# Kernel tuning notes

Measured on AMD Instinct MI355X. Metric: run time of the kernel, lower is better.

## Reference

```python
import jax, jax.numpy as jnp
import numpy as np

CUTOFFS = [16000, 28000, 36000]
HID = 1024
PROJ = [256, 64]  # hidden/4**1, hidden/4**2 per compute_proj_dims
CLUSTERS = 2


def setup_inputs() -> dict:
    key = jax.random.key(0)
    ks = jax.random.split(key, 12)
    B, S = 4, 1024
    scale = 0.02
    d = {
        "inp": jax.random.normal(ks[0], (B, S, HID), jnp.float32),
        "labels": jax.random.randint(ks[1], (B, S), 0, CUTOFFS[-1]),
        "head_W": jax.random.normal(ks[2], (HID, CUTOFFS[0] + CLUSTERS), jnp.float32) * scale,
        "head_b": jnp.zeros((CUTOFFS[0] + CLUSTERS,), jnp.float32),
    }
    for i in range(CLUSTERS):
        tdim = CUTOFFS[i + 1] - CUTOFFS[i]
        d[f"t{i}_pW"] = jax.random.normal(ks[3 + 4 * i], (HID, PROJ[i]), jnp.float32) * scale
        d[f"t{i}_pb"] = jnp.zeros((PROJ[i],), jnp.float32)
        d[f"t{i}_W"] = jax.random.normal(ks[4 + 4 * i], (PROJ[i], CUTOFFS[i + 1] - CUTOFFS[i]), jnp.float32) * scale
        d[f"t{i}_b"] = jnp.zeros((CUTOFFS[i + 1] - CUTOFFS[i],), jnp.float32)
    return d


def _sparse_ce(logits, labels):
    # stable sparse softmax cross entropy, single log_softmax pass
    logp = jax.nn.log_softmax(logits, axis=-1)
    return -jnp.take_along_axis(logp, labels[..., None], axis=-1)[..., 0]


def reference(inp, labels, head_W, head_b, t0_pW, t0_pb, t0_W, t0_b, t1_pW, t1_pb, t1_W, t1_b):
    tails = [(t0_pW, t0_pb, t0_W, t0_b), (t1_pW, t1_pb, t1_W, t1_b)]
    head_labels = labels
    loss = jnp.zeros(labels.shape, inp.dtype)
    for i, (pW, pb, W, b) in enumerate(tails):
        lo, hi = CUTOFFS[i], CUTOFFS[i + 1]
        mask = (labels >= lo) & (labels < hi)
        # tokens in cluster i are relabeled to cluster id in the head
        head_labels = jnp.where(mask, CUTOFFS[0] + i, head_labels)
        # two-layer tail projection: [B,S,H] -> [B,S,proj] -> [B,S,tail_dim]
        tail_logits = (inp @ pW + pb) @ W + b
        tail_labels = jnp.clip(labels - lo, 0, hi - lo - 1)
        loss = loss + jnp.where(mask, _sparse_ce(tail_logits, tail_labels), 0.0)
    head_logits = inp @ head_W + head_b  # [B,S,cutoffs[0]+clusters]
    loss = _sparse_ce(head_logits, head_labels) + loss
    loss = loss * (labels != 0).astype(loss.dtype)  # zero out pad positions
    return jnp.mean(loss)
```

## Files before the change

kernel.cpp:

```cpp
#include <hip/hip_runtime.h>
#include <hip/hip_bf16.h>
#include <hip/hip_fp8.h>
#include <cstdint>
#include <cstddef>

#define M_TOK 4096
#define HID   1024
#define NHEAD 16002
#define NHEAD_PAD 16128
#define P0    256
#define N0    12000
#define N0_PAD 12032
#define P1    64
#define N1    8000
#define N1_PAD 8192
#define PFUSE 384
#define PREAL 320

typedef unsigned char u8;
typedef float f32x4 __attribute__((ext_vector_type(4)));
typedef int   i32x4 __attribute__((ext_vector_type(4)));
typedef int   i32x8 __attribute__((ext_vector_type(8)));

__device__ __forceinline__ void load16(const void* g, void* l) {
    __builtin_amdgcn_global_load_lds(
        (__attribute__((address_space(1))) void*)g,
        (__attribute__((address_space(3))) void*)l,
        16, 0, 0);
}

__device__ __forceinline__ u8 to_e4m3(float f) {
    __hip_fp8_e4m3 h(f);
    return (u8)h.__x;
}

union Frag { struct { i32x4 lo, hi; } half; i32x8 v; };

struct Seg {
    const u8* A; int lda;
    const u8* BT; int ldb;
    const float* bias; int K; int realN;
    const int* tgt; float* sumexp; float* lab;
    int nblk;
};

__launch_bounds__(512, 4)
__global__ void gemm_lse3(Seg s0, Seg s1, Seg s2) {
    __shared__ __align__(16) u8 As[32768];
    __shared__ __align__(16) u8 Bs[16384];

    int b = blockIdx.x;
    Seg sg; int rel;
    if (b < s0.nblk)                { sg = s0; rel = b; }
    else if (b < s0.nblk + s1.nblk) { sg = s1; rel = b - s0.nblk; }
    else                            { sg = s2; rel = b - s0.nblk - s1.nblk; }
    int pair = rel >> 5, inner = rel & 31;
    int m0 = (inner >> 1) * 256;
    int n0 = (pair * 2 + (inner & 1)) * 128;

    const int lda = sg.lda, ldb = sg.ldb;
    const int tid  = threadIdx.x;
    const int lane = tid & 63;
    const int wave = tid >> 6;
    const int wm = wave >> 1, wn = wave & 1;
    const int q = lane >> 4, lrow = lane & 15;
    const int sw = lrow & 7;

    int aofs[4], abase[4], bofs[2], bbase[2];
    #pragma unroll
    for (int p = 0; p < 4; p++) {
        int pg = wave * 256 + p * 64 + lane;
        int row = pg >> 3, gcol = (pg & 7) ^ (row & 7);
        aofs[p]  = row * lda + gcol * 16;
        abase[p] = (wave * 256 + p * 64) * 16;
    }
    #pragma unroll
    for (int p = 0; p < 2; p++) {
        int pg = wave * 128 + p * 64 + lane;
        int row = pg >> 3, gcol = (pg & 7) ^ (row & 7);
        bofs[p]  = row * ldb + gcol * 16;
        bbase[p] = (wave * 128 + p * 64) * 16;
    }

    f32x4 acc[4][4];
    #pragma unroll
    for (int mt = 0; mt < 4; mt++)
        #pragma unroll
        for (int nt = 0; nt < 4; nt++)
            acc[mt][nt] = (f32x4)(0.0f);

    const u8* Ab = sg.A  + (size_t)m0 * lda;
    const u8* Bb = sg.BT + (size_t)n0 * ldb;

    const int aLo = ((wm * 64 + lrow) * 8 + ((2 * q)     ^ sw)) * 16;
    const int aHi = ((wm * 64 + lrow) * 8 + ((2 * q + 1) ^ sw)) * 16;
    const int bLo = ((wn * 64 + lrow) * 8 + ((2 * q)     ^ sw)) * 16;
    const int bHi = ((wn * 64 + lrow) * 8 + ((2 * q + 1) ^ sw)) * 16;

    for (int k0 = 0; k0 < sg.K; k0 += 128) {
        #pragma unroll
        for (int p = 0; p < 4; p++)
            load16(Ab + k0 + aofs[p], As + abase[p]);
        #pragma unroll
        for (int p = 0; p < 2; p++)
            load16(Bb + k0 + bofs[p], Bs + bbase[p]);
        __syncthreads();

        Frag fb[4];
        #pragma unroll
        for (int t = 0; t < 4; t++) {
            fb[t].half.lo = *reinterpret_cast<const i32x4*>(Bs + bLo + t * 2048);
            fb[t].half.hi = *reinterpret_cast<const i32x4*>(Bs + bHi + t * 2048);
        }
        Frag fa[2];
        fa[0].half.lo = *reinterpret_cast<const i32x4*>(As + aLo);
        fa[0].half.hi = *reinterpret_cast<const i32x4*>(As + aHi);
        #pragma unroll
        for (int mt = 0; mt < 4; mt++) {
            if (mt < 3) {
                fa[(mt + 1) & 1].half.lo = *reinterpret_cast<const i32x4*>(As + aLo + (mt + 1) * 2048);
                fa[(mt + 1) & 1].half.hi = *reinterpret_cast<const i32x4*>(As + aHi + (mt + 1) * 2048);
            }
            #pragma unroll
            for (int nt = 0; nt < 4; nt++)
                acc[mt][nt] = __builtin_amdgcn_mfma_scale_f32_16x16x128_f8f6f4(
                    fa[mt & 1].v, fb[nt].v, acc[mt][nt],
                    0, 0,
                    0, 0x7F7F7F7F,
                    0, 0x7A7A7A7A);
        }
        __syncthreads();
    }

    int colg[4]; float bias_v[4];
    #pragma unroll
    for (int nt = 0; nt < 4; nt++) {
        colg[nt] = n0 + wn * 64 + nt * 16 + lrow;
        bias_v[nt] = (colg[nt] < sg.realN) ? sg.bias[colg[nt]] : 0.0f;
    }

    float* sred = reinterpret_cast<float*>(As);

    #pragma unroll
    for (int mt = 0; mt < 4; mt++) {
        int rloc = wm * 64 + mt * 16 + q * 4;
        #pragma unroll
        for (int r = 0; r < 4; r++) {
            int tok = m0 + rloc + r;
            int tg = sg.tgt[tok];
            float ps = 0.0f;
            #pragma unroll
            for (int nt = 0; nt < 4; nt++) {
                if (colg[nt] < sg.realN) {
                    float logit = acc[mt][nt][r] + bias_v[nt];
                    ps += __expf(logit);
                    if (colg[nt] == tg) atomicAdd(&sg.lab[tok], logit);
                }
            }
            ps += __shfl_xor(ps, 1);
            ps += __shfl_xor(ps, 2);
            ps += __shfl_xor(ps, 4);
            ps += __shfl_xor(ps, 8);
            if (lrow == 0) sred[wn * 256 + rloc + r] = ps;
        }
    }
    __syncthreads();
    if (tid < 256) {
        float v = sred[tid] + sred[256 + tid];
        atomicAdd(&sg.sumexp[m0 + tid], v);
    }
}

__device__ __forceinline__ void proj_body(const u8* __restrict__ A, const u8* __restrict__ BT,
                                          const float* __restrict__ bias, u8* __restrict__ out,
                                          int m0, int n0, u8* As, u8* Bs) {
    const int lda = HID, ldb = HID, ldo = PFUSE;
    const int tid  = threadIdx.x;
    const int lane = tid & 63;
    const int wave = tid >> 6;
    const int wm = wave >> 2, wn = wave & 3;
    const int q = lane >> 4, lrow = lane & 15;
    const int sw = lrow & 7;

    int aofs[2], bofs[2], lbase[2];
    #pragma unroll
    for (int p = 0; p < 2; p++) {
        int pg = wave * 128 + p * 64 + lane;
        int row = pg >> 3, gcol = (pg & 7) ^ (row & 7);
        aofs[p]  = row * lda + gcol * 16;
        bofs[p]  = row * ldb + gcol * 16;
        lbase[p] = (wave * 128 + p * 64) * 16;
    }

    f32x4 acc[4][2];
    #pragma unroll
    for (int mt = 0; mt < 4; mt++)
        #pragma unroll
        for (int nt = 0; nt < 2; nt++)
            acc[mt][nt] = (f32x4)(0.0f);

    const u8* Ab = A  + (size_t)m0 * lda;
    const u8* Bb = BT + (size_t)n0 * ldb;

    const int aLo = ((wm * 64 + lrow) * 8 + ((2 * q)     ^ sw)) * 16;
    const int aHi = ((wm * 64 + lrow) * 8 + ((2 * q + 1) ^ sw)) * 16;
    const int bLo = ((wn * 32 + lrow) * 8 + ((2 * q)     ^ sw)) * 16;
    const int bHi = ((wn * 32 + lrow) * 8 + ((2 * q + 1) ^ sw)) * 16;

    for (int k0 = 0; k0 < HID; k0 += 128) {
        #pragma unroll
        for (int p = 0; p < 2; p++) {
            load16(Ab + k0 + aofs[p], As + lbase[p]);
            load16(Bb + k0 + bofs[p], Bs + lbase[p]);
        }
        __syncthreads();
        Frag fb[2];
        #pragma unroll
        for (int t = 0; t < 2; t++) {
            fb[t].half.lo = *reinterpret_cast<const i32x4*>(Bs + bLo + t * 2048);
            fb[t].half.hi = *reinterpret_cast<const i32x4*>(Bs + bHi + t * 2048);
        }
        #pragma unroll
        for (int mt = 0; mt < 4; mt++) {
            Frag fa;
            fa.half.lo = *reinterpret_cast<const i32x4*>(As + aLo + mt * 2048);
            fa.half.hi = *reinterpret_cast<const i32x4*>(As + aHi + mt * 2048);
            #pragma unroll
            for (int nt = 0; nt < 2; nt++)
                acc[mt][nt] = __builtin_amdgcn_mfma_scale_f32_16x16x128_f8f6f4(
                    fa.v, fb[nt].v, acc[mt][nt],
                    0, 0, 0, 0x7F7F7F7F, 0, 0x7A7A7A7A);
        }
        __syncthreads();
    }

    int colg[2]; float bias_v[2];
    #pragma unroll
    for (int nt = 0; nt < 2; nt++) {
        colg[nt] = n0 + wn * 32 + nt * 16 + lrow;
        bias_v[nt] = (colg[nt] < PREAL) ? bias[colg[nt]] : 0.0f;
    }
    #pragma unroll
    for (int mt = 0; mt < 4; mt++) {
        int rowb = m0 + wm * 64 + mt * 16 + q * 4;
        #pragma unroll
        for (int r = 0; r < 4; r++) {
            int tok = rowb + r;
            #pragma unroll
            for (int nt = 0; nt < 2; nt++)
                out[(size_t)tok * ldo + colg[nt]] = to_e4m3(acc[mt][nt][r] + bias_v[nt]);
        }
    }
}

__device__ __forceinline__ void do_transpose512(const float* __restrict__ W, u8* __restrict__ WT,
                                                int K, int N, int Kpad, float scale,
                                                int bx, int by, float (*tile)[65]) {
    int n0 = bx * 64, k0 = by * 64;
    int c2 = threadIdx.x & 31;
    int rg = threadIdx.x >> 5;
    int n = n0 + c2 * 2;
    #pragma unroll
    for (int j = 0; j < 4; j++) {
        int k = k0 + rg + j * 16;
        float2 v;
        if (k < K && n + 1 < N) {
            v = *reinterpret_cast<const float2*>(&W[(size_t)k * N + n]);
        } else {
            v.x = (k < K && n     < N) ? W[(size_t)k * N + n]     : 0.0f;
            v.y = (k < K && n + 1 < N) ? W[(size_t)k * N + n + 1] : 0.0f;
        }
        tile[rg + j * 16][c2 * 2]     = v.x * scale;
        tile[rg + j * 16][c2 * 2 + 1] = v.y * scale;
    }
    __syncthreads();
    int nn = threadIdx.x >> 3, kb = (threadIdx.x & 7) * 8;
    union { u8 b[8]; uint2 u; } v;
    #pragma unroll
    for (int j = 0; j < 8; j++) v.b[j] = to_e4m3(tile[kb + j][nn]);
    *reinterpret_cast<uint2*>(WT + (size_t)(n0 + nn) * Kpad + k0 + kb) = v.u;
}

#define P1_CAST 512
#define P1_T0P   64
#define P1_T1P   32
#define P1_INIT   8

__global__ void prep1_kernel(const float* __restrict__ inp, const int* __restrict__ labels,
                             const float* __restrict__ t0_pW, const float* __restrict__ t0_pb,
                             const float* __restrict__ t1_pW, const float* __restrict__ t1_pb,
                             u8* __restrict__ inp_f8, u8* __restrict__ fpW8,
                             float* __restrict__ acc6, int* __restrict__ tgts,
                             float* __restrict__ pbias, float* __restrict__ out) {
    __shared__ float tile[64][65];
    int b = blockIdx.x;
    if (b < P1_CAST) {
        int i = b * 512 + threadIdx.x;
        float4 v = reinterpret_cast<const float4*>(inp)[i];
        uchar4 o8;
        o8.x = to_e4m3(v.x); o8.y = to_e4m3(v.y); o8.z = to_e4m3(v.z); o8.w = to_e4m3(v.w);
        reinterpret_cast<uchar4*>(inp_f8)[i] = o8;
    } else if (b < P1_CAST + P1_T0P) {
        int r = b - P1_CAST;
        do_transpose512(t0_pW, fpW8, HID, P0, HID, 32.0f, r % 4, r / 4, tile);
    } else if (b < P1_CAST + P1_T0P + P1_T1P) {
        int r = b - (P1_CAST + P1_T0P);
        do_transpose512(t1_pW, fpW8 + 256 * HID, HID, P1, HID, 32.0f, r % 2, r / 2, tile);
    } else {
        int r = b - (P1_CAST + P1_T0P + P1_T1P);
        int t = r * 512 + threadIdx.x;
        for (int j = t; j < 6 * M_TOK; j += M_TOK) acc6[j] = 0.0f;
        if (t == 0) out[0] = 0.0f;
        if (t < PFUSE) pbias[t] = (t < 256) ? t0_pb[t] : ((t < PREAL) ? t1_pb[t - 256] : 0.0f);
        int lbl = labels[t];
        tgts[t]             = (lbl < 16000) ? lbl : ((lbl < 28000) ? 16000 : 16001);
        int t0 = lbl - 16000; t0 = t0 < 0 ? 0 : (t0 > 11999 ? 11999 : t0);
        int t1 = lbl - 28000; t1 = t1 < 0 ? 0 : (t1 > 7999  ? 7999  : t1);
        tgts[M_TOK + t]     = t0;
        tgts[2 * M_TOK + t] = t1;
    }
}

#define P2_HEAD 4032
#define P2_T0W   752
#define P2_T1W   256
#define P2_PROJ   96

__launch_bounds__(512, 4)
__global__ void prep2_kernel(const float* __restrict__ head_W,
                             const float* __restrict__ t0_W, const float* __restrict__ t1_W,
                             const u8* __restrict__ inp_f8, const u8* __restrict__ fpW8,
                             const float* __restrict__ pbias,
                             u8* __restrict__ headW8, u8* __restrict__ t0W8,
                             u8* __restrict__ t1W8, u8* __restrict__ proj8) {
    __shared__ __align__(16) u8 smem[32768];
    int b = blockIdx.x;
    if (b < P2_HEAD) {
        do_transpose512(head_W, headW8, HID, NHEAD, HID, 32.0f, b % 252, b / 252,
                        reinterpret_cast<float (*)[65]>(smem));
    } else if (b < P2_HEAD + P2_T0W) {
        int r = b - P2_HEAD;
        do_transpose512(t0_W, t0W8, P0, N0, P0, 32.0f, r % 188, r / 188,
                        reinterpret_cast<float (*)[65]>(smem));
    } else if (b < P2_HEAD + P2_T0W + P2_T1W) {
        int r = b - (P2_HEAD + P2_T0W);
        do_transpose512(t1_W, t1W8, P1, N1, 128, 32.0f, r % 128, r / 128,
                        reinterpret_cast<float (*)[65]>(smem));
    } else {
        int r = b - (P2_HEAD + P2_T0W + P2_T1W);
        int m0 = (r & 31) * 128;
        int n0 = (r >> 5) * 128;
        proj_body(inp_f8, fpW8, pbias, proj8, m0, n0, smem, smem + 16384);
    }
}

__global__ void finalize_kernel(const int* __restrict__ labels, const float* __restrict__ acc6,
                                float* __restrict__ out) {
    int t = blockIdx.x * blockDim.x + threadIdx.x;
    const float* sumH = acc6;
    const float* labH = acc6 + M_TOK;
    const float* sum0 = acc6 + 2 * M_TOK;
    const float* lab0 = acc6 + 3 * M_TOK;
    const float* sum1 = acc6 + 4 * M_TOK;
    const float* lab1 = acc6 + 5 * M_TOK;
    int lbl = labels[t];
    float l = 0.0f;
    if (lbl != 0) {
        l = logf(sumH[t]) - labH[t];
        if (lbl >= 16000 && lbl < 28000) l += logf(sum0[t]) - lab0[t];
        else if (lbl >= 28000)           l += logf(sum1[t]) - lab1[t];
    }
    l *= (1.0f / (float)M_TOK);
    #pragma unroll
    for (int off = 1; off < 64; off <<= 1) l += __shfl_xor(l, off);
    __shared__ float red[4];
    if ((threadIdx.x & 63) == 0) red[threadIdx.x >> 6] = l;
    __syncthreads();
    if (threadIdx.x == 0) atomicAdd(out, red[0] + red[1] + red[2] + red[3]);
}

extern "C" void kernel_launch(void* const* d_in, const int* in_sizes, int n_in,
                              void* d_out, int out_size, void* d_ws, size_t ws_size,
                              hipStream_t stream) {
    const float* inp    = (const float*)d_in[0];
    const int*   labels = (const int*)  d_in[1];
    const float* head_W = (const float*)d_in[2];
    const float* head_b = (const float*)d_in[3];
    const float* t0_pW  = (const float*)d_in[4];
    const float* t0_pb  = (const float*)d_in[5];
    const float* t0_W   = (const float*)d_in[6];
    const float* t0_b   = (const float*)d_in[7];
    const float* t1_pW  = (const float*)d_in[8];
    const float* t1_pb  = (const float*)d_in[9];
    const float* t1_W   = (const float*)d_in[10];
    const float* t1_b   = (const float*)d_in[11];
    float* out = (float*)d_out;

    char* ws = (char*)d_ws;
    size_t off = 0;
    auto alloc = [&](size_t bytes) { char* p = ws + off; off += (bytes + 255) & ~(size_t)255; return p; };
    u8*    inp_f8  = (u8*)   alloc((size_t)M_TOK * HID);
    u8*    headW8  = (u8*)   alloc((size_t)NHEAD_PAD * HID);
    u8*    fpW8    = (u8*)   alloc((size_t)PFUSE * HID);
    u8*    t0W8    = (u8*)   alloc((size_t)N0_PAD * P0);
    u8*    t1W8    = (u8*)   alloc((size_t)N1_PAD * 128);
    u8*    proj8   = (u8*)   alloc((size_t)M_TOK * PFUSE);
    float* acc6    = (float*)alloc(6 * M_TOK * 4);
    int*   tgts    = (int*)  alloc(3 * M_TOK * 4);
    float* pbias   = (float*)alloc(PFUSE * 4);

    prep1_kernel<<<P1_CAST + P1_T0P + P1_T1P + P1_INIT, 512, 0, stream>>>(
        inp, labels, t0_pW, t0_pb, t1_pW, t1_pb,
        inp_f8, fpW8, acc6, tgts, pbias, out);

    prep2_kernel<<<P2_HEAD + P2_T0W + P2_T1W + P2_PROJ, 512, 0, stream>>>(
        head_W, t0_W, t1_W, inp_f8, fpW8, pbias,
        headW8, t0W8, t1W8, proj8);

    Seg s0{inp_f8,      HID,   headW8, HID, head_b, HID, NHEAD, tgts,             acc6,             acc6 + M_TOK,     16 * (NHEAD_PAD / 128)};
    Seg s1{proj8,       PFUSE, t0W8,   P0,  t0_b,   P0,  N0,    tgts + M_TOK,     acc6 + 2 * M_TOK, acc6 + 3 * M_TOK, 16 * (N0_PAD / 128)};
    Seg s2{proj8 + 256, PFUSE, t1W8,   128, t1_b,   128, N1,    tgts + 2 * M_TOK, acc6 + 4 * M_TOK, acc6 + 5 * M_TOK, 16 * (N1_PAD / 128)};
    gemm_lse3<<<s0.nblk + s1.nblk + s2.nblk, 512, 0, stream>>>(s0, s1, s2);

    finalize_kernel<<<M_TOK / 256, 256, 0, stream>>>(labels, acc6, out);
}
```

Before: 301.5 us.

## Fuse finalize into GEMM via last-block reduction and use packed fp8 conversion

The separate finalize kernel is removed. Each GEMM block now bumps a global counter after its atomics, and whichever block finishes last computes the loss reduction and writes the output. The transpose-and-cast helper now converts to fp8 before staging through LDS, using packed hardware cvt_pk_fp8 intrinsics, with larger tiles of 128 k by 64 n and half the block count. This aims to save one kernel launch and cut LDS traffic and conversion instructions in the prep kernels, at the cost of a fence plus a global atomic per GEMM block.

After: 897.9 us. 2.98x slower.

```diff
diff --git a/kernel.cpp b/kernel.cpp
--- a/kernel.cpp
+++ b/kernel.cpp
@@ -1,6 +1,5 @@
 #include <hip/hip_runtime.h>
 #include <hip/hip_bf16.h>
-#include <hip/hip_fp8.h>
 #include <cstdint>
 #include <cstddef>
 
@@ -30,8 +29,16 @@
 }
 
 __device__ __forceinline__ u8 to_e4m3(float f) {
-    __hip_fp8_e4m3 h(f);
-    return (u8)h.__x;
+    return (u8)(__builtin_amdgcn_cvt_pk_fp8_f32(f, f, 0, false) & 0xff);
+}
+__device__ __forceinline__ unsigned cvt4(float x, float y, float z, float w) {
+    int r = __builtin_amdgcn_cvt_pk_fp8_f32(x, y, 0, false);
+    r = __builtin_amdgcn_cvt_pk_fp8_f32(z, w, r, true);
+    return (unsigned)r;
+}
+
+__device__ __forceinline__ float aload(const float* p) {
+    return __hip_atomic_load(p, __ATOMIC_RELAXED, __HIP_MEMORY_SCOPE_AGENT);
 }
 
 union Frag { struct { i32x4 lo, hi; } half; i32x8 v; };
@@ -45,7 +52,9 @@
 };
 
 __launch_bounds__(512, 4)
-__global__ void gemm_lse3(Seg s0, Seg s1, Seg s2) {
+__global__ void gemm_lse3(Seg s0, Seg s1, Seg s2,
+                          const int* __restrict__ labels, float* __restrict__ acc6,
+                          int* __restrict__ cnt, float* __restrict__ out, int nblkTotal) {
     __shared__ __align__(16) u8 As[32768];
     __shared__ __align__(16) u8 Bs[16384];
 
@@ -169,6 +178,40 @@
         float v = sred[tid] + sred[256 + tid];
         atomicAdd(&sg.sumexp[m0 + tid], v);
     }
+
+    __threadfence();
+    __shared__ int lastBlk;
+    __syncthreads();
+    if (tid == 0) {
+        int old = __hip_atomic_fetch_add(cnt, 1, __ATOMIC_ACQ_REL, __HIP_MEMORY_SCOPE_AGENT);
+        lastBlk = (old == nblkTotal - 1) ? 1 : 0;
+    }
+    __syncthreads();
+    if (lastBlk) {
+        float part = 0.0f;
+        for (int t = tid; t < M_TOK; t += 512) {
+            int lbl = labels[t];
+            if (lbl != 0) {
+                float l = logf(aload(&acc6[t])) - aload(&acc6[M_TOK + t]);
+                if (lbl >= 16000 && lbl < 28000)
+                    l += logf(aload(&acc6[2 * M_TOK + t])) - aload(&acc6[3 * M_TOK + t]);
+                else if (lbl >= 28000)
+                    l += logf(aload(&acc6[4 * M_TOK + t])) - aload(&acc6[5 * M_TOK + t]);
+                part += l;
+            }
+        }
+        #pragma unroll
+        for (int o = 1; o < 64; o <<= 1) part += __shfl_xor(part, o);
+        float* red = reinterpret_cast<float*>(Bs);
+        if ((tid & 63) == 0) red[tid >> 6] = part;
+        __syncthreads();
+        if (tid == 0) {
+            float s = 0.0f;
+            #pragma unroll
+            for (int i = 0; i < 8; i++) s += red[i];
+            out[0] = s * (1.0f / (float)M_TOK);
+        }
+    }
 }
 
 __device__ __forceinline__ void proj_body(const u8* __restrict__ A, const u8* __restrict__ BT,
@@ -253,37 +296,44 @@
     }
 }
 
-__device__ __forceinline__ void do_transpose512(const float* __restrict__ W, u8* __restrict__ WT,
-                                                int K, int N, int Kpad, float scale,
-                                                int bx, int by, float (*tile)[65]) {
-    int n0 = bx * 64, k0 = by * 64;
-    int c2 = threadIdx.x & 31;
-    int rg = threadIdx.x >> 5;
-    int n = n0 + c2 * 2;
+__device__ __forceinline__ void tr_cast(const float* __restrict__ W, u8* __restrict__ WT,
+                                        int K, int N, int Kpad, float scale,
+                                        int bx, int by, u8* ldsb ) {
+    int n0 = bx * 64, k0 = by * 128;
+    int c4 = threadIdx.x & 15;
+    int rg = threadIdx.x >> 4;
+    int n = n0 + c4 * 4;
     #pragma unroll
     for (int j = 0; j < 4; j++) {
-        int k = k0 + rg + j * 16;
-        float2 v;
-        if (k < K && n + 1 < N) {
-            v = *reinterpret_cast<const float2*>(&W[(size_t)k * N + n]);
-        } else {
-            v.x = (k < K && n     < N) ? W[(size_t)k * N + n]     : 0.0f;
-            v.y = (k < K && n + 1 < N) ? W[(size_t)k * N + n + 1] : 0.0f;
-        }
-        tile[rg + j * 16][c2 * 2]     = v.x * scale;
-        tile[rg + j * 16][c2 * 2 + 1] = v.y * scale;
+        int kr = rg + j * 32;
+        int k = k0 + kr;
+        float2 v01 = make_float2(0.f, 0.f), v23 = make_float2(0.f, 0.f);
+        if (k < K) {
+            const float* row = W + (size_t)k * N;
+            if (n + 3 < N) {
+                v01 = *reinterpret_cast<const float2*>(row + n);
+                v23 = *reinterpret_cast<const float2*>(row + n + 2);
+            } else {
+                if (n     < N) v01.x = row[n];
+                if (n + 1 < N) v01.y = row[n + 1];
+                if (n + 2 < N) v23.x = row[n + 2];
+                if (n + 3 < N) v23.y = row[n + 3];
+            }
+        }
+        unsigned pk = cvt4(v01.x * scale, v01.y * scale, v23.x * scale, v23.y * scale);
+        *reinterpret_cast<unsigned*>(ldsb + kr * 68 + c4 * 4) = pk;
     }
     __syncthreads();
-    int nn = threadIdx.x >> 3, kb = (threadIdx.x & 7) * 8;
-    union { u8 b[8]; uint2 u; } v;
-    #pragma unroll
-    for (int j = 0; j < 8; j++) v.b[j] = to_e4m3(tile[kb + j][nn]);
-    *reinterpret_cast<uint2*>(WT + (size_t)(n0 + nn) * Kpad + k0 + kb) = v.u;
-}
-
-#define P1_CAST 512
-#define P1_T0P   64
-#define P1_T1P   32
+    int nn = threadIdx.x >> 3, kb = (threadIdx.x & 7) * 16;
+    union { u8 b[16]; uint4 u; } o;
+    #pragma unroll
+    for (int j = 0; j < 16; j++) o.b[j] = ldsb[(kb + j) * 68 + nn];
+    *reinterpret_cast<uint4*>(WT + (size_t)(n0 + nn) * Kpad + k0 + kb) = o.u;
+}
+
+#define P1_CAST 256
+#define P1_T0P   32
+#define P1_T1P   16
 #define P1_INIT   8
 
 __global__ void prep1_kernel(const float* __restrict__ inp, const int* __restrict__ labels,
@@ -291,26 +341,28 @@
                              const float* __restrict__ t1_pW, const float* __restrict__ t1_pb,
                              u8* __restrict__ inp_f8, u8* __restrict__ fpW8,
                              float* __restrict__ acc6, int* __restrict__ tgts,
-                             float* __restrict__ pbias, float* __restrict__ out) {
-    __shared__ float tile[64][65];
+                             float* __restrict__ pbias, int* __restrict__ cnt,
+                             float* __restrict__ out) {
+    __shared__ __align__(16) u8 ldsb[128 * 68];
     int b = blockIdx.x;
     if (b < P1_CAST) {
-        int i = b * 512 + threadIdx.x;
-        float4 v = reinterpret_cast<const float4*>(inp)[i];
-        uchar4 o8;
-        o8.x = to_e4m3(v.x); o8.y = to_e4m3(v.y); o8.z = to_e4m3(v.z); o8.w = to_e4m3(v.w);
-        reinterpret_cast<uchar4*>(inp_f8)[i] = o8;
+        #pragma unroll
+        for (int h = 0; h < 2; h++) {
+            int i = b * 1024 + h * 512 + threadIdx.x;
+            float4 v = reinterpret_cast<const float4*>(inp)[i];
+            reinterpret_cast<unsigned*>(inp_f8)[i] = cvt4(v.x, v.y, v.z, v.w);
+        }
     } else if (b < P1_CAST + P1_T0P) {
         int r = b - P1_CAST;
-        do_transpose512(t0_pW, fpW8, HID, P0, HID, 32.0f, r % 4, r / 4, tile);
+        tr_cast(t0_pW, fpW8, HID, P0, HID, 32.0f, r & 3, r >> 2, ldsb);
     } else if (b < P1_CAST + P1_T0P + P1_T1P) {
         int r = b - (P1_CAST + P1_T0P);
-        do_transpose512(t1_pW, fpW8 + 256 * HID, HID, P1, HID, 32.0f, r % 2, r / 2, tile);
+        tr_cast(t1_pW, fpW8 + 256 * HID, HID, P1, HID, 32.0f, r & 1, r >> 1, ldsb);
     } else {
         int r = b - (P1_CAST + P1_T0P + P1_T1P);
         int t = r * 512 + threadIdx.x;
         for (int j = t; j < 6 * M_TOK; j += M_TOK) acc6[j] = 0.0f;
-        if (t == 0) out[0] = 0.0f;
+        if (t == 0) { out[0] = 0.0f; cnt[0] = 0; }
         if (t < PFUSE) pbias[t] = (t < 256) ? t0_pb[t] : ((t < PREAL) ? t1_pb[t - 256] : 0.0f);
         int lbl = labels[t];
         tgts[t]             = (lbl < 16000) ? lbl : ((lbl < 28000) ? 16000 : 16001);
@@ -321,9 +373,9 @@
     }
 }
 
-#define P2_HEAD 4032
-#define P2_T0W   752
-#define P2_T1W   256
+#define P2_HEAD 2016
+#define P2_T0W   376
+#define P2_T1W   128
 #define P2_PROJ   96
 
 __launch_bounds__(512, 4)
@@ -336,47 +388,19 @@
     __shared__ __align__(16) u8 smem[32768];
     int b = blockIdx.x;
     if (b < P2_HEAD) {
-        do_transpose512(head_W, headW8, HID, NHEAD, HID, 32.0f, b % 252, b / 252,
-                        reinterpret_cast<float (*)[65]>(smem));
+        tr_cast(head_W, headW8, HID, NHEAD, HID, 32.0f, b % 252, b / 252, smem);
     } else if (b < P2_HEAD + P2_T0W) {
         int r = b - P2_HEAD;
-        do_transpose512(t0_W, t0W8, P0, N0, P0, 32.0f, r % 188, r / 188,
-                        reinterpret_cast<float (*)[65]>(smem));
+        tr_cast(t0_W, t0W8, P0, N0, P0, 32.0f, r % 188, r / 188, smem);
     } else if (b < P2_HEAD + P2_T0W + P2_T1W) {
         int r = b - (P2_HEAD + P2_T0W);
-        do_transpose512(t1_W, t1W8, P1, N1, 128, 32.0f, r % 128, r / 128,
-                        reinterpret_cast<float (*)[65]>(smem));
+        tr_cast(t1_W, t1W8, P1, N1, 128, 32.0f, r, 0, smem);
     } else {
         int r = b - (P2_HEAD + P2_T0W + P2_T1W);
         int m0 = (r & 31) * 128;
         int n0 = (r >> 5) * 128;
         proj_body(inp_f8, fpW8, pbias, proj8, m0, n0, smem, smem + 16384);
     }
-}
-
-__global__ void finalize_kernel(const int* __restrict__ labels, const float* __restrict__ acc6,
-                                float* __restrict__ out) {
-    int t = blockIdx.x * blockDim.x + threadIdx.x;
-    const float* sumH = acc6;
-    const float* labH = acc6 + M_TOK;
-    const float* sum0 = acc6 + 2 * M_TOK;
-    const float* lab0 = acc6 + 3 * M_TOK;
-    const float* sum1 = acc6 + 4 * M_TOK;
-    const float* lab1 = acc6 + 5 * M_TOK;
-    int lbl = labels[t];
-    float l = 0.0f;
-    if (lbl != 0) {
-        l = logf(sumH[t]) - labH[t];
-        if (lbl >= 16000 && lbl < 28000) l += logf(sum0[t]) - lab0[t];
-        else if (lbl >= 28000)           l += logf(sum1[t]) - lab1[t];
-    }
-    l *= (1.0f / (float)M_TOK);
-    #pragma unroll
-    for (int off = 1; off < 64; off <<= 1) l += __shfl_xor(l, off);
-    __shared__ float red[4];
-    if ((threadIdx.x & 63) == 0) red[threadIdx.x >> 6] = l;
-    __syncthreads();
-    if (threadIdx.x == 0) atomicAdd(out, red[0] + red[1] + red[2] + red[3]);
 }
 
 extern "C" void kernel_launch(void* const* d_in, const int* in_sizes, int n_in,
@@ -408,10 +432,11 @@
     float* acc6    = (float*)alloc(6 * M_TOK * 4);
     int*   tgts    = (int*)  alloc(3 * M_TOK * 4);
     float* pbias   = (float*)alloc(PFUSE * 4);
+    int*   cnt     = (int*)  alloc(256);
 
     prep1_kernel<<<P1_CAST + P1_T0P + P1_T1P + P1_INIT, 512, 0, stream>>>(
         inp, labels, t0_pW, t0_pb, t1_pW, t1_pb,
-        inp_f8, fpW8, acc6, tgts, pbias, out);
+        inp_f8, fpW8, acc6, tgts, pbias, cnt, out);
 
     prep2_kernel<<<P2_HEAD + P2_T0W + P2_T1W + P2_PROJ, 512, 0, stream>>>(
         head_W, t0_W, t1_W, inp_f8, fpW8, pbias,
@@ -420,7 +445,6 @@
     Seg s0{inp_f8,      HID,   headW8, HID, head_b, HID, NHEAD, tgts,             acc6,             acc6 + M_TOK,     16 * (NHEAD_PAD / 128)};
     Seg s1{proj8,       PFUSE, t0W8,   P0,  t0_b,   P0,  N0,    tgts + M_TOK,     acc6 + 2 * M_TOK, acc6 + 3 * M_TOK, 16 * (N0_PAD / 128)};
     Seg s2{proj8 + 256, PFUSE, t1W8,   128, t1_b,   128, N1,    tgts + 2 * M_TOK, acc6 + 4 * M_TOK, acc6 + 5 * M_TOK, 16 * (N1_PAD / 128)};
-    gemm_lse3<<<s0.nblk + s1.nblk + s2.nblk, 512, 0, stream>>>(s0, s1, s2);
-
-    finalize_kernel<<<M_TOK / 256, 256, 0, stream>>>(labels, acc6, out);
-}
+    int nblkTotal = s0.nblk + s1.nblk + s2.nblk;
+    gemm_lse3<<<nblkTotal, 512, 0, stream>>>(s0, s1, s2, labels, acc6, cnt, out, nblkTotal);
+}
```
